# Performance work log

Measured on AMD Instinct MI355X. Metric: run time of the kernel, lower is better.

Reference implementation:

```python
import jax, jax.numpy as jnp
import numpy as np

N_ENTRIES = 4_194_304   # total CSR entries (gene observations)
H, W = 256, 256
N_PIXELS = H * W
N_GENES = 30000
FEATURE_DIM = 64


def setup_inputs() -> dict:
    key = jax.random.key(0)
    k1, k2, k3, k4 = jax.random.split(key, 4)
    # gene id per CSR entry
    indices = jax.random.randint(k1, (N_ENTRIES,), 0, N_GENES, dtype=jnp.int64)
    # counts per entry (positive floats)
    cnts = jax.random.uniform(k2, (N_ENTRIES,), dtype=jnp.float32) * 10.0
    # CSR row pointers over pixels: sorted, starting at 0, ending at N_ENTRIES
    indptr = jnp.sort(jax.random.randint(k3, (N_PIXELS + 1,), 0, N_ENTRIES + 1, dtype=jnp.int64))
    indptr = indptr.at[0].set(0).at[-1].set(N_ENTRIES)
    # params: gamma init zeros, tokens variance_scaling(1.0,'fan_in','normal',out_axis=0)
    gamma = jnp.zeros((N_GENES,), jnp.float32)
    tokens = jax.random.normal(k4, (N_GENES, FEATURE_DIM), dtype=jnp.float32) * (1.0 / np.sqrt(FEATURE_DIM))
    return {"indices": indices, "cnts": cnts, "indptr": indptr, "gamma": gamma, "tokens": tokens}


def reference(indices, cnts, indptr, gamma, tokens):
    # SGStem with rescale=True, normalize=False (module defaults)
    n_entries = indices.shape[0]
    n_pixels = indptr.shape[0] - 1  # == H*W
    # mask padding entries beyond indptr[-1]
    valid = jnp.arange(n_entries) < indptr[-1]
    c = jnp.where(valid, cnts, 0.0)
    # rescale counts by per-gene exp(gamma)
    c = c * jnp.exp(gamma[indices])
    # CSR -> segment ids per entry
    rpt = jnp.diff(indptr)
    segms = jnp.repeat(jnp.arange(n_pixels), rpt, total_repeat_length=n_entries)
    # gather token embeddings, scale, scatter-add into pixel bins
    embeddings = tokens[indices] * c[:, None]  # (n_entries, feature_dim)
    embedding_sum = jax.ops.segment_sum(embeddings, segms, num_segments=n_pixels)
    return embedding_sum.reshape(H, W, tokens.shape[-1])
```

## Files before the change

kernel.cpp:

```cpp
#include <hip/hip_runtime.h>
#include <hip/hip_bf16.h>

#define FDIM 64
#define N_PIXELS 65536
#define N_ENTRIES 4194304
#define N_GENES 30000
#define WAVES_PER_BLOCK 4
#define N_WAVES 8192
#define EPW (N_ENTRIES / N_WAVES)

__device__ __forceinline__ unsigned short f32_to_bf16_rne(float f) {
    unsigned int u = __float_as_uint(f);
    u = (u + 0x7FFFu + ((u >> 16) & 1u)) >> 16;
    return (unsigned short)u;
}

__global__ __launch_bounds__(256) void convert_tokens(
    const float4* __restrict__ tokens4,
    ushort4* __restrict__ tok_bf)
{
    const int i = blockIdx.x * blockDim.x + threadIdx.x;
    const float4 t = tokens4[i];
    ushort4 o;
    o.x = f32_to_bf16_rne(t.x);
    o.y = f32_to_bf16_rne(t.y);
    o.z = f32_to_bf16_rne(t.z);
    o.w = f32_to_bf16_rne(t.w);
    tok_bf[i] = o;
}

__global__ __launch_bounds__(WAVES_PER_BLOCK * 64) void sgstem_main(
    const int* __restrict__ indices,
    const float* __restrict__ cnts,
    const int* __restrict__ indptr,
    const float* __restrict__ gamma,
    const uint4* __restrict__ tok_bf,
    float* __restrict__ out)
{
    __shared__ int2 meta[WAVES_PER_BLOCK][64];

    const int lane = threadIdx.x & 63;
    const int wave = threadIdx.x >> 6;
    const int g    = lane >> 3;
    const int fl   = lane & 7;

    const int wid = __builtin_amdgcn_readfirstlane(
        blockIdx.x * WAVES_PER_BLOCK + wave);
    const int e0 = wid * EPW;
    const int e1 = e0 + EPW;

    int lo = 0, hi = N_PIXELS;
    while (lo < hi) {
        const int mid = (lo + hi + 1) >> 1;
        if (indptr[mid] <= e0) lo = mid; else hi = mid - 1;
    }
    int p = lo;

    while (p < N_PIXELS) {
        const int ps = indptr[p];
        if (ps >= e1) break;
        const int pe = indptr[p + 1];
        const int s = max(ps, e0);
        const int t = min(pe, e1);

        if (t > s) {
            float a0 = 0.f, a1 = 0.f, a2 = 0.f, a3 = 0.f;
            float a4 = 0.f, a5 = 0.f, a6 = 0.f, a7 = 0.f;

            for (int base = s; base < t; base += 64) {
                const int e = base + lane;
                int   idx   = 0;
                float scale = 0.0f;
                if (e < t) {
                    idx   = indices[e];
                    scale = cnts[e] * __expf(gamma[idx]);
                }
                int2 mt;
                mt.x = idx;
                mt.y = __float_as_int(scale);
                meta[wave][lane] = mt;

                const int m = t - base;
                const int niter = (m >= 64) ? 8 : ((m + 7) >> 3);
                #pragma unroll 4
                for (int j = 0; j < niter; ++j) {
                    const int2 mm = meta[wave][j * 8 + g];
                    const float sc = __int_as_float(mm.y);
                    const uint4 tk = tok_bf[mm.x * 8 + fl];
                    a0 = fmaf(__uint_as_float(tk.x << 16), sc, a0);
                    a1 = fmaf(__uint_as_float(tk.x & 0xFFFF0000u), sc, a1);
                    a2 = fmaf(__uint_as_float(tk.y << 16), sc, a2);
                    a3 = fmaf(__uint_as_float(tk.y & 0xFFFF0000u), sc, a3);
                    a4 = fmaf(__uint_as_float(tk.z << 16), sc, a4);
                    a5 = fmaf(__uint_as_float(tk.z & 0xFFFF0000u), sc, a5);
                    a6 = fmaf(__uint_as_float(tk.w << 16), sc, a6);
                    a7 = fmaf(__uint_as_float(tk.w & 0xFFFF0000u), sc, a7);
                }
            }

            #pragma unroll
            for (int mask = 8; mask <= 32; mask <<= 1) {
                a0 += __shfl_xor(a0, mask);
                a1 += __shfl_xor(a1, mask);
                a2 += __shfl_xor(a2, mask);
                a3 += __shfl_xor(a3, mask);
                a4 += __shfl_xor(a4, mask);
                a5 += __shfl_xor(a5, mask);
                a6 += __shfl_xor(a6, mask);
                a7 += __shfl_xor(a7, mask);
            }

            if (g == 0) {
                const bool interior = (ps >= e0) && (pe <= e1);
                if (interior) {
                    float4* o4 = (float4*)(out + p * FDIM);
                    o4[fl * 2]     = make_float4(a0, a1, a2, a3);
                    o4[fl * 2 + 1] = make_float4(a4, a5, a6, a7);
                } else {
                    float* o = out + p * FDIM + fl * 8;
                    atomicAdd(o + 0, a0);
                    atomicAdd(o + 1, a1);
                    atomicAdd(o + 2, a2);
                    atomicAdd(o + 3, a3);
                    atomicAdd(o + 4, a4);
                    atomicAdd(o + 5, a5);
                    atomicAdd(o + 6, a6);
                    atomicAdd(o + 7, a7);
                }
            }
        }
        ++p;
    }
}

extern "C" void kernel_launch(void* const* d_in, const int* in_sizes, int n_in,
                              void* d_out, int out_size, void* d_ws, size_t ws_size,
                              hipStream_t stream) {
    const int*    indices = (const int*)d_in[0];
    const float*  cnts    = (const float*)d_in[1];
    const int*    indptr  = (const int*)d_in[2];
    const float*  gamma   = (const float*)d_in[3];
    const float4* tokens4 = (const float4*)d_in[4];
    float*        out     = (float*)d_out;

    ushort4* tok_bf = (ushort4*)d_ws;

    hipMemsetAsync(d_out, 0, (size_t)N_PIXELS * FDIM * sizeof(float), stream);

    convert_tokens<<<1875, 256, 0, stream>>>(tokens4, tok_bf);

    sgstem_main<<<N_WAVES / WAVES_PER_BLOCK, WAVES_PER_BLOCK * 64, 0, stream>>>(
        indices, cnts, indptr, gamma, (const uint4*)tok_bf, out);
}
```

Before: 162.3 us.

## Fold exp(gamma) into bf16 tokens and prestage per-wave metadata in LDS

Moves the per-gene exp(gamma) scaling into the token conversion kernel, which removes a dependent gamma gather and exp from each entry in the main kernel. Each wave now loads all 512 of its indices and counts into shared memory once at the start, instead of reloading metadata for every 64-entry chunk of each pixel. The inner loop is unrolled to issue four independent token gathers per iteration, with clamped LDS indices and zeroed scales for out-of-range lanes. Shared memory use grows to 16 KB per block and a minimum-occupancy launch bound is added, which may raise register pressure. Baking the scale in before bf16 rounding also changes the numerics slightly.

```diff
diff --git a/kernel.cpp b/kernel.cpp
--- a/kernel.cpp
+++ b/kernel.cpp
@@ -7,7 +7,7 @@
 #define N_GENES 30000
 #define WAVES_PER_BLOCK 4
 #define N_WAVES 8192
-#define EPW (N_ENTRIES / N_WAVES)
+#define EPW 512
 
 __device__ __forceinline__ unsigned short f32_to_bf16_rne(float f) {
     unsigned int u = __float_as_uint(f);
@@ -17,27 +17,29 @@
 
 __global__ __launch_bounds__(256) void convert_tokens(
     const float4* __restrict__ tokens4,
+    const float* __restrict__ gamma,
     ushort4* __restrict__ tok_bf)
 {
     const int i = blockIdx.x * blockDim.x + threadIdx.x;
+    const int g = i >> 4;
+    const float eg = __expf(gamma[g]);
     const float4 t = tokens4[i];
     ushort4 o;
-    o.x = f32_to_bf16_rne(t.x);
-    o.y = f32_to_bf16_rne(t.y);
-    o.z = f32_to_bf16_rne(t.z);
-    o.w = f32_to_bf16_rne(t.w);
+    o.x = f32_to_bf16_rne(t.x * eg);
+    o.y = f32_to_bf16_rne(t.y * eg);
+    o.z = f32_to_bf16_rne(t.z * eg);
+    o.w = f32_to_bf16_rne(t.w * eg);
     tok_bf[i] = o;
 }
 
-__global__ __launch_bounds__(WAVES_PER_BLOCK * 64) void sgstem_main(
+__global__ __launch_bounds__(WAVES_PER_BLOCK * 64, 8) void sgstem_main(
     const int* __restrict__ indices,
     const float* __restrict__ cnts,
     const int* __restrict__ indptr,
-    const float* __restrict__ gamma,
     const uint4* __restrict__ tok_bf,
     float* __restrict__ out)
 {
-    __shared__ int2 meta[WAVES_PER_BLOCK][64];
+    __shared__ int2 meta[WAVES_PER_BLOCK][EPW];
 
     const int lane = threadIdx.x & 63;
     const int wave = threadIdx.x >> 6;
@@ -48,6 +50,14 @@
         blockIdx.x * WAVES_PER_BLOCK + wave);
     const int e0 = wid * EPW;
     const int e1 = e0 + EPW;
+
+    #pragma unroll
+    for (int c = 0; c < 8; ++c) {
+        const int e = e0 + c * 64 + lane;
+        const int   idx = indices[e];
+        const float cnt = cnts[e];
+        meta[wave][c * 64 + lane] = make_int2(idx * 8, __float_as_int(cnt));
+    }
 
     int lo = 0, hi = N_PIXELS;
     while (lo < hi) {
@@ -64,38 +74,65 @@
         const int t = min(pe, e1);
 
         if (t > s) {
+            const int r0 = s - e0;
+            const int r1 = t - e0;
+
             float a0 = 0.f, a1 = 0.f, a2 = 0.f, a3 = 0.f;
             float a4 = 0.f, a5 = 0.f, a6 = 0.f, a7 = 0.f;
 
-            for (int base = s; base < t; base += 64) {
-                const int e = base + lane;
-                int   idx   = 0;
-                float scale = 0.0f;
-                if (e < t) {
-                    idx   = indices[e];
-                    scale = cnts[e] * __expf(gamma[idx]);
-                }
-                int2 mt;
-                mt.x = idx;
-                mt.y = __float_as_int(scale);
-                meta[wave][lane] = mt;
+            for (int rb = r0; rb < r1; rb += 32) {
+                const int q0 = rb + g;
+                const int q1 = q0 + 8;
+                const int q2 = q0 + 16;
+                const int q3 = q0 + 24;
+                const int2 m0 = meta[wave][min(q0, EPW - 1)];
+                const int2 m1 = meta[wave][min(q1, EPW - 1)];
+                const int2 m2 = meta[wave][min(q2, EPW - 1)];
+                const int2 m3 = meta[wave][min(q3, EPW - 1)];
+                const uint4 t0 = tok_bf[m0.x + fl];
+                const uint4 t1 = tok_bf[m1.x + fl];
+                const uint4 t2 = tok_bf[m2.x + fl];
+                const uint4 t3 = tok_bf[m3.x + fl];
+                const float s0 = (q0 < r1) ? __int_as_float(m0.y) : 0.f;
+                const float s1 = (q1 < r1) ? __int_as_float(m1.y) : 0.f;
+                const float s2 = (q2 < r1) ? __int_as_float(m2.y) : 0.f;
+                const float s3 = (q3 < r1) ? __int_as_float(m3.y) : 0.f;
 
-                const int m = t - base;
-                const int niter = (m >= 64) ? 8 : ((m + 7) >> 3);
-                #pragma unroll 4
-                for (int j = 0; j < niter; ++j) {
-                    const int2 mm = meta[wave][j * 8 + g];
-                    const float sc = __int_as_float(mm.y);
-                    const uint4 tk = tok_bf[mm.x * 8 + fl];
-                    a0 = fmaf(__uint_as_float(tk.x << 16), sc, a0);
-                    a1 = fmaf(__uint_as_float(tk.x & 0xFFFF0000u), sc, a1);
-                    a2 = fmaf(__uint_as_float(tk.y << 16), sc, a2);
-                    a3 = fmaf(__uint_as_float(tk.y & 0xFFFF0000u), sc, a3);
-                    a4 = fmaf(__uint_as_float(tk.z << 16), sc, a4);
-                    a5 = fmaf(__uint_as_float(tk.z & 0xFFFF0000u), sc, a5);
-                    a6 = fmaf(__uint_as_float(tk.w << 16), sc, a6);
-                    a7 = fmaf(__uint_as_float(tk.w & 0xFFFF0000u), sc, a7);
-                }
+                a0 = fmaf(__uint_as_float(t0.x << 16),        s0, a0);
+                a1 = fmaf(__uint_as_float(t0.x & 0xFFFF0000u), s0, a1);
+                a2 = fmaf(__uint_as_float(t0.y << 16),        s0, a2);
+                a3 = fmaf(__uint_as_float(t0.y & 0xFFFF0000u), s0, a3);
+                a4 = fmaf(__uint_as_float(t0.z << 16),        s0, a4);
+                a5 = fmaf(__uint_as_float(t0.z & 0xFFFF0000u), s0, a5);
+                a6 = fmaf(__uint_as_float(t0.w << 16),        s0, a6);
+                a7 = fmaf(__uint_as_float(t0.w & 0xFFFF0000u), s0, a7);
+
+                a0 = fmaf(__uint_as_float(t1.x << 16),        s1, a0);
+                a1 = fmaf(__uint_as_float(t1.x & 0xFFFF0000u), s1, a1);
+                a2 = fmaf(__uint_as_float(t1.y << 16),        s1, a2);
+                a3 = fmaf(__uint_as_float(t1.y & 0xFFFF0000u), s1, a3);
+                a4 = fmaf(__uint_as_float(t1.z << 16),        s1, a4);
+                a5 = fmaf(__uint_as_float(t1.z & 0xFFFF0000u), s1, a5);
+                a6 = fmaf(__uint_as_float(t1.w << 16),        s1, a6);
+                a7 = fmaf(__uint_as_float(t1.w & 0xFFFF0000u), s1, a7);
+
+                a0 = fmaf(__uint_as_float(t2.x << 16),        s2, a0);
+                a1 = fmaf(__uint_as_float(t2.x & 0xFFFF0000u), s2, a1);
+                a2 = fmaf(__uint_as_float(t2.y << 16),        s2, a2);
+                a3 = fmaf(__uint_as_float(t2.y & 0xFFFF0000u), s2, a3);
+                a4 = fmaf(__uint_as_float(t2.z << 16),        s2, a4);
+                a5 = fmaf(__uint_as_float(t2.z & 0xFFFF0000u), s2, a5);
+                a6 = fmaf(__uint_as_float(t2.w << 16),        s2, a6);
+                a7 = fmaf(__uint_as_float(t2.w & 0xFFFF0000u), s2, a7);
+
+                a0 = fmaf(__uint_as_float(t3.x << 16),        s3, a0);
+                a1 = fmaf(__uint_as_float(t3.x & 0xFFFF0000u), s3, a1);
+                a2 = fmaf(__uint_as_float(t3.y << 16),        s3, a2);
+                a3 = fmaf(__uint_as_float(t3.y & 0xFFFF0000u), s3, a3);
+                a4 = fmaf(__uint_as_float(t3.z << 16),        s3, a4);
+                a5 = fmaf(__uint_as_float(t3.z & 0xFFFF0000u), s3, a5);
+                a6 = fmaf(__uint_as_float(t3.w << 16),        s3, a6);
+                a7 = fmaf(__uint_as_float(t3.w & 0xFFFF0000u), s3, a7);
             }
 
             #pragma unroll
@@ -147,8 +184,8 @@
 
     hipMemsetAsync(d_out, 0, (size_t)N_PIXELS * FDIM * sizeof(float), stream);
 
-    convert_tokens<<<1875, 256, 0, stream>>>(tokens4, tok_bf);
+    convert_tokens<<<1875, 256, 0, stream>>>(tokens4, gamma, tok_bf);
 
     sgstem_main<<<N_WAVES / WAVES_PER_BLOCK, WAVES_PER_BLOCK * 64, 0, stream>>>(
-        indices, cnts, indptr, gamma, (const uint4*)tok_bf, out);
+        indices, cnts, indptr, (const uint4*)tok_bf, out);
 }
```

Result: faster. 145.7 us (-10.2%).
